# Kernel optimization log

Measured on AMD Instinct MI355X. Metric: run time of the kernel, lower is better.

Reference implementation:

```python
import jax, jax.numpy as jnp
import numpy as np

N = 8192


def setup_inputs() -> dict:
    key = jax.random.key(0)
    k1, k2 = jax.random.split(key)
    X = jax.random.normal(k1, (N,), dtype=jnp.float32)
    X_hat = jax.random.normal(k2, (N,), dtype=jnp.float32)
    return {"X": X, "X_hat": X_hat}


def reference(X, X_hat):
    n = X.shape[0]
    # Faithful to the torch module: compare argsort indices (not ranks)
    # over the full i,j meshgrid ('ij' indexing == broadcasting below).
    a = jnp.argsort(X)        # [n] int
    b = jnp.argsort(X_hat)    # [n] int
    ai, aj = a[:, None], a[None, :]   # [n,1], [1,n]
    bi, bj = b[:, None], b[None, :]
    disordered = ((ai < aj) & (bi > bj)) | ((ai > aj) & (bi < bj))  # [n,n] bool
    ndisordered = jnp.sum(disordered)
    return ndisordered.astype(jnp.float32) / (n * (n - 1))
```

## Files before the change

### kernel.cpp

```cpp
#include <hip/hip_runtime.h>

#define KN 8192

__device__ __forceinline__ unsigned long long make_key(float x, int idx) {
    unsigned int u = __float_as_uint(x);
    u ^= (unsigned int)((int)u >> 31) | 0x80000000u;
    return ((unsigned long long)u << 13) | (unsigned int)idx;
}

constexpr int UT  = 1024;
constexpr int VC  = 256;
constexpr int NVT = KN / VC;

__global__ __launch_bounds__(256) void rank_partial(const float* __restrict__ X,
                                                    const float* __restrict__ Xh,
                                                    int* __restrict__ part) {
    int blk = blockIdx.x;
    int arr = blk & 1;
    int vt  = (blk >> 1) & (NVT - 1);
    int ut  = blk >> 6;
    const float* src = arr ? Xh : X;

    int tid = threadIdx.x;
    int u0 = ut * UT + tid;

    unsigned long long ku0 = make_key(src[u0],       u0);
    unsigned long long ku1 = make_key(src[u0 + 256], u0 + 256);
    unsigned long long ku2 = make_key(src[u0 + 512], u0 + 512);
    unsigned long long ku3 = make_key(src[u0 + 768], u0 + 768);

    __shared__ __align__(16) unsigned long long tile[VC];
    {
        int v = vt * VC + tid;
        tile[tid] = make_key(src[v], v);
    }
    __syncthreads();

    const ulonglong2* t2 = (const ulonglong2*)tile;
    int c0 = 0, c1 = 0, c2 = 0, c3 = 0;
#pragma unroll 8
    for (int j = 0; j < VC / 2; ++j) {
        ulonglong2 kv = t2[j];
        c0 += (kv.x < ku0) + (kv.y < ku0);
        c1 += (kv.x < ku1) + (kv.y < ku1);
        c2 += (kv.x < ku2) + (kv.y < ku2);
        c3 += (kv.x < ku3) + (kv.y < ku3);
    }

    int base = (arr * NVT + vt) * KN + u0;
    part[base]       = c0;
    part[base + 256] = c1;
    part[base + 512] = c2;
    part[base + 768] = c3;
}

__global__ __launch_bounds__(256) void reduce_scatter(const int* __restrict__ part,
                                                      int* __restrict__ a,
                                                      int* __restrict__ b,
                                                      unsigned long long* __restrict__ acc) {
    int t = blockIdx.x * 256 + threadIdx.x;
    if (t == 0) *acc = 0ULL;
    int arr = t >> 13;
    int u   = t & (KN - 1);

    const int* p = part + (arr * NVT) * KN + u;
    int r = 0;
#pragma unroll
    for (int vt = 0; vt < NVT; ++vt) r += p[vt * KN];

    if (arr == 0) a[r] = u; else b[r] = u;
}

constexpr int KT    = 1024;
constexpr int LT    = 128;
constexpr int NLT   = KN / LT;
constexpr int NBLK3 = (KN / KT) * NLT;

__global__ __launch_bounds__(256) void pair_count(const int* __restrict__ a,
                                                  const int* __restrict__ b,
                                                  unsigned long long* __restrict__ acc,
                                                  float* __restrict__ out) {
    int blk = blockIdx.x;
    int lt  = blk & (NLT - 1);
    int kt  = blk >> 6;
    int tid = threadIdx.x;

    __shared__ int2 tl[LT];
    __shared__ int wsum[4];
    if (tid < LT) {
        int l = lt * LT + tid;
        tl[tid] = make_int2(a[l], b[l]);
    }
    int k0  = kt * KT + tid;
    int ak0 = a[k0], ak1 = a[k0 + 256], ak2 = a[k0 + 512], ak3 = a[k0 + 768];
    int bk0 = b[k0], bk1 = b[k0 + 256], bk2 = b[k0 + 512], bk3 = b[k0 + 768];
    __syncthreads();

    int c = 0;
#pragma unroll 8
    for (int j = 0; j < LT; ++j) {
        int2 v = tl[j];
        c += (ak0 < v.x) != (bk0 < v.y);
        c += (ak1 < v.x) != (bk1 < v.y);
        c += (ak2 < v.x) != (bk2 < v.y);
        c += (ak3 < v.x) != (bk3 < v.y);
    }

    for (int off = 32; off; off >>= 1) c += __shfl_down(c, off);
    if ((tid & 63) == 0) wsum[tid >> 6] = c;
    __syncthreads();
    if (tid == 0) {
        unsigned long long partial =
            (unsigned long long)(wsum[0] + wsum[1] + wsum[2] + wsum[3]);
        unsigned long long old = atomicAdd(acc, (1ULL << 40) | partial);
        if ((old >> 40) == (unsigned long long)(NBLK3 - 1)) {
            unsigned long long total = (old & ((1ULL << 40) - 1)) + partial;
            out[0] = (float)total / 67100672.0f;
        }
    }
}

extern "C" void kernel_launch(void* const* d_in, const int* in_sizes, int n_in,
                              void* d_out, int out_size, void* d_ws, size_t ws_size,
                              hipStream_t stream) {
    const float* X  = (const float*)d_in[0];
    const float* Xh = (const float*)d_in[1];

    char* ws = (char*)d_ws;
    int* part = (int*)(ws);
    int* a    = (int*)(ws + 2097152);
    int* b    = (int*)(ws + 2129920);
    unsigned long long* acc = (unsigned long long*)(ws + 2162688);

    rank_partial  <<<dim3(512), dim3(256), 0, stream>>>(X, Xh, part);
    reduce_scatter<<<dim3(64),  dim3(256), 0, stream>>>(part, a, b, acc);
    pair_count    <<<dim3(512), dim3(256), 0, stream>>>(a, b, acc, (float*)d_out);
}
```

Measured before the change: 81.54 us.

## Exploit pair symmetry in pair_count and halve rank_partial per-thread keys

pair_count now walks only the upper-triangular tile pairs (528 blocks of 256x256), counting strict j>i inside diagonal tiles and doubling the total at the end, so roughly half the pairwise comparisons are skipped. rank_partial drops from four keys per thread to two and launches twice as many blocks, trading per-thread reuse of the shared tile for more parallelism. The triangular index decode uses a serial loop per block, and diagonal tiles have an uneven per-thread loop.

```diff
diff --git a/kernel.cpp b/kernel.cpp
--- a/kernel.cpp
+++ b/kernel.cpp
@@ -8,7 +8,7 @@
     return ((unsigned long long)u << 13) | (unsigned int)idx;
 }
 
-constexpr int UT  = 1024;
+constexpr int UT  = 512;
 constexpr int VC  = 256;
 constexpr int NVT = KN / VC;
 
@@ -26,8 +26,6 @@
 
     unsigned long long ku0 = make_key(src[u0],       u0);
     unsigned long long ku1 = make_key(src[u0 + 256], u0 + 256);
-    unsigned long long ku2 = make_key(src[u0 + 512], u0 + 512);
-    unsigned long long ku3 = make_key(src[u0 + 768], u0 + 768);
 
     __shared__ __align__(16) unsigned long long tile[VC];
     {
@@ -37,21 +35,17 @@
     __syncthreads();
 
     const ulonglong2* t2 = (const ulonglong2*)tile;
-    int c0 = 0, c1 = 0, c2 = 0, c3 = 0;
+    int c0 = 0, c1 = 0;
 #pragma unroll 8
     for (int j = 0; j < VC / 2; ++j) {
         ulonglong2 kv = t2[j];
         c0 += (kv.x < ku0) + (kv.y < ku0);
         c1 += (kv.x < ku1) + (kv.y < ku1);
-        c2 += (kv.x < ku2) + (kv.y < ku2);
-        c3 += (kv.x < ku3) + (kv.y < ku3);
     }
 
     int base = (arr * NVT + vt) * KN + u0;
     part[base]       = c0;
     part[base + 256] = c1;
-    part[base + 512] = c2;
-    part[base + 768] = c3;
 }
 
 __global__ __launch_bounds__(256) void reduce_scatter(const int* __restrict__ part,
@@ -71,39 +65,43 @@
     if (arr == 0) a[r] = u; else b[r] = u;
 }
 
-constexpr int KT    = 1024;
-constexpr int LT    = 128;
-constexpr int NLT   = KN / LT;
-constexpr int NBLK3 = (KN / KT) * NLT;
+constexpr int TS    = 256;
+constexpr int T     = KN / TS;
+constexpr int NBLK3 = T * (T + 1) / 2;
 
 __global__ __launch_bounds__(256) void pair_count(const int* __restrict__ a,
                                                   const int* __restrict__ b,
                                                   unsigned long long* __restrict__ acc,
                                                   float* __restrict__ out) {
     int blk = blockIdx.x;
-    int lt  = blk & (NLT - 1);
-    int kt  = blk >> 6;
+    int p = 0, rem = blk;
+    while (rem >= T - p) { rem -= T - p; ++p; }
+    int q = p + rem;
     int tid = threadIdx.x;
 
-    __shared__ int2 tl[LT];
+    __shared__ __align__(16) int2 tl[TS];
     __shared__ int wsum[4];
-    if (tid < LT) {
-        int l = lt * LT + tid;
-        tl[tid] = make_int2(a[l], b[l]);
-    }
-    int k0  = kt * KT + tid;
-    int ak0 = a[k0], ak1 = a[k0 + 256], ak2 = a[k0 + 512], ak3 = a[k0 + 768];
-    int bk0 = b[k0], bk1 = b[k0 + 256], bk2 = b[k0 + 512], bk3 = b[k0 + 768];
+
+    int k  = p * TS + tid;
+    int ak = a[k], bk = b[k];
+    int l  = q * TS + tid;
+    tl[tid] = make_int2(a[l], b[l]);
     __syncthreads();
 
     int c = 0;
+    if (p == q) {
+        for (int j = tid + 1; j < TS; ++j) {
+            int2 v = tl[j];
+            c += (ak < v.x) != (bk < v.y);
+        }
+    } else {
+        const int4* t4 = (const int4*)tl;
 #pragma unroll 8
-    for (int j = 0; j < LT; ++j) {
-        int2 v = tl[j];
-        c += (ak0 < v.x) != (bk0 < v.y);
-        c += (ak1 < v.x) != (bk1 < v.y);
-        c += (ak2 < v.x) != (bk2 < v.y);
-        c += (ak3 < v.x) != (bk3 < v.y);
+        for (int j = 0; j < TS / 2; ++j) {
+            int4 v = t4[j];
+            c += (ak < v.x) != (bk < v.y);
+            c += (ak < v.z) != (bk < v.w);
+        }
     }
 
     for (int off = 32; off; off >>= 1) c += __shfl_down(c, off);
@@ -114,8 +112,8 @@
             (unsigned long long)(wsum[0] + wsum[1] + wsum[2] + wsum[3]);
         unsigned long long old = atomicAdd(acc, (1ULL << 40) | partial);
         if ((old >> 40) == (unsigned long long)(NBLK3 - 1)) {
-            unsigned long long total = (old & ((1ULL << 40) - 1)) + partial;
-            out[0] = (float)total / 67100672.0f;
+            unsigned long long D = (old & ((1ULL << 40) - 1)) + partial;
+            out[0] = (float)(2ULL * D) / 67100672.0f;
         }
     }
 }
@@ -132,7 +130,7 @@
     int* b    = (int*)(ws + 2129920);
     unsigned long long* acc = (unsigned long long*)(ws + 2162688);
 
-    rank_partial  <<<dim3(512), dim3(256), 0, stream>>>(X, Xh, part);
-    reduce_scatter<<<dim3(64),  dim3(256), 0, stream>>>(part, a, b, acc);
-    pair_count    <<<dim3(512), dim3(256), 0, stream>>>(a, b, acc, (float*)d_out);
+    rank_partial  <<<dim3(1024), dim3(256), 0, stream>>>(X, Xh, part);
+    reduce_scatter<<<dim3(64),   dim3(256), 0, stream>>>(part, a, b, acc);
+    pair_count    <<<dim3(528),  dim3(256), 0, stream>>>(a, b, acc, (float*)d_out);
 }
```

Result: faster. 78.53 us (-3.7%).
